# Kernel tuning notes

Measured on AMD Instinct MI355X. Metric: run time of the kernel, lower is better.

## Reference

```python
import jax, jax.numpy as jnp
import numpy as np

D_MODEL = 1024
NUM_HEADS = 16
DEPTH = D_MODEL // NUM_HEADS
B, S = 4, 2048


def setup_inputs() -> dict:
    key = jax.random.key(0)
    ks = jax.random.split(key, 11)
    sc = 1.0 / np.sqrt(D_MODEL)
    return {
        "query": jax.random.normal(ks[0], (B, S, D_MODEL), jnp.float32),
        "key_": jax.random.normal(ks[1], (B, S, D_MODEL), jnp.float32),
        "value": jax.random.normal(ks[2], (B, S, D_MODEL), jnp.float32),
        # torch Linear: y = x @ W.T + b, W shape [out, in]
        "Wq": jax.random.normal(ks[3], (D_MODEL, D_MODEL), jnp.float32) * sc,
        "bq": jax.random.normal(ks[4], (D_MODEL,), jnp.float32) * sc,
        "Wk": jax.random.normal(ks[5], (D_MODEL, D_MODEL), jnp.float32) * sc,
        "bk": jax.random.normal(ks[6], (D_MODEL,), jnp.float32) * sc,
        "Wv": jax.random.normal(ks[7], (D_MODEL, D_MODEL), jnp.float32) * sc,
        "bv": jax.random.normal(ks[8], (D_MODEL,), jnp.float32) * sc,
        "Wo": jax.random.normal(ks[9], (D_MODEL, D_MODEL), jnp.float32) * sc,
        "bo": jax.random.normal(ks[10], (D_MODEL,), jnp.float32) * sc,
    }


def _split_heads(x):
    # [B,S,D] -> [B,H,S,depth]
    b, s, _ = x.shape
    return x.reshape(b, s, NUM_HEADS, DEPTH).transpose(0, 2, 1, 3)


def reference(query, key_, value, Wq, bq, Wk, bk, Wv, bv, Wo, bo):
    Q = _split_heads(query @ Wq.T + bq)
    K = _split_heads(key_ @ Wk.T + bk)
    V = _split_heads(value @ Wv.T + bv)
    scale = 1.0 / jnp.sqrt(jnp.float32(DEPTH))
    scores = jnp.einsum("bhqd,bhkd->bhqk", Q, K) * scale  # [B,H,S,S]
    attention_weights = jax.nn.softmax(scores, axis=-1)
    out = jnp.einsum("bhqk,bhkd->bhqd", attention_weights, V)
    out = out.transpose(0, 2, 1, 3).reshape(query.shape[0], -1, D_MODEL)
    out = out @ Wo.T + bo
    return out, attention_weights
```

## Files before the change

kernel.cpp:

```cpp
#include <hip/hip_runtime.h>

#define NHEAD 16
#define SEQ 2048
#define DMODEL 1024
#define BB 4
#define MROWS (BB*SEQ)
#define NBH (BB*NHEAD)
#define NT (SEQ/32)

typedef float f32x4 __attribute__((ext_vector_type(4)));
typedef _Float16 f16x8 __attribute__((ext_vector_type(8)));
typedef _Float16 f16x4 __attribute__((ext_vector_type(4)));

static __device__ __forceinline__ f32x4 mfma16(f16x8 a, f16x8 b, f32x4 c) {
  return __builtin_amdgcn_mfma_f32_16x16x32_f16(a, b, c, 0, 0, 0);
}

static __device__ __forceinline__ void gload_lds16(const unsigned short* g, unsigned short* l) {
  __builtin_amdgcn_global_load_lds(
      (const __attribute__((address_space(1))) unsigned int*)g,
      (__attribute__((address_space(3))) unsigned int*)l, 16, 0, 0);
}

static __device__ __forceinline__ ushort4 cvt4(float4 x) {
  ushort4 h;
  h.x = __builtin_bit_cast(unsigned short, (_Float16)x.x);
  h.y = __builtin_bit_cast(unsigned short, (_Float16)x.y);
  h.z = __builtin_bit_cast(unsigned short, (_Float16)x.z);
  h.w = __builtin_bit_cast(unsigned short, (_Float16)x.w);
  return h;
}

__global__ __launch_bounds__(256)
void round3_f16(const float* __restrict__ q, const float* __restrict__ k,
                const float* __restrict__ v,
                unsigned short* __restrict__ oq, unsigned short* __restrict__ ok,
                unsigned short* __restrict__ ov, int n4)
{
  const float* src = (blockIdx.y == 0) ? q : (blockIdx.y == 1) ? k : v;
  unsigned short* dst = (blockIdx.y == 0) ? oq : (blockIdx.y == 1) ? ok : ov;
  int i = blockIdx.x*256 + threadIdx.x;
  const int stride = gridDim.x*256;
  for (; i < n4; i += stride)
    ((ushort4*)dst)[i] = cvt4(((const float4*)src)[i]);
}

__global__ __launch_bounds__(256)
void round_w4(const float* __restrict__ w0, const float* __restrict__ w1,
              const float* __restrict__ w2, const float* __restrict__ w3,
              unsigned short* __restrict__ o0, unsigned short* __restrict__ o1,
              unsigned short* __restrict__ o2, unsigned short* __restrict__ o3, int n4)
{
  const float* src = (blockIdx.y == 0) ? w0 : (blockIdx.y == 1) ? w1
                   : (blockIdx.y == 2) ? w2 : w3;
  unsigned short* dst = (blockIdx.y == 0) ? o0 : (blockIdx.y == 1) ? o1
                      : (blockIdx.y == 2) ? o2 : o3;
  int i = blockIdx.x*256 + threadIdx.x;
  const int stride = gridDim.x*256;
  for (; i < n4; i += stride)
    ((ushort4*)dst)[i] = cvt4(((const float4*)src)[i]);
}

static __device__ __forceinline__ void stage_proj(
    unsigned short* ab, unsigned short* bb,
    const unsigned short* __restrict__ Xf, const unsigned short* __restrict__ Wf,
    int m0, int n0, int k0, int tid)
{
#pragma unroll
  for (int r = 0; r < 2; ++r) {
    const int gi = r*256 + tid;
    const int row = gi >> 2, c = gi & 3;
    const int lg = c ^ ((row >> 1) & 3);
    gload_lds16(Xf + (size_t)(m0+row)*DMODEL + k0 + lg*8,
                ab + r*2048 + (tid & 0xC0)*8);
  }
#pragma unroll
  for (int r = 0; r < 2; ++r) {
    const int gi = r*256 + tid;
    const int row = gi >> 2, c = gi & 3;
    const int lg = c ^ ((row >> 1) & 3);
    gload_lds16(Wf + (size_t)(n0+row)*DMODEL + k0 + lg*8,
                bb + r*2048 + (tid & 0xC0)*8);
  }
}

template<int MODE>
__global__ __launch_bounds__(256, 2)
void proj_gemm(const unsigned short* __restrict__ Xf, const unsigned short* __restrict__ Wf,
               const float* __restrict__ bias, float oscale,
               unsigned short* __restrict__ o16, float* __restrict__ o_f32)
{
  __shared__ unsigned short As[2][128][32];
  __shared__ unsigned short Bs[2][128][32];
  const int tid  = threadIdx.x;
  const int wid  = tid >> 6, lane = tid & 63;
  const int g    = lane >> 4, r16 = lane & 15;
  const int id   = blockIdx.y*64 + blockIdx.x;
  const int xcd  = id & 7, slot = id >> 3;
  const int m0   = (xcd*8 + (slot & 7)) * 128;
  const int n0   = (slot >> 3) * 128;
  const int wr   = wid >> 1, wc = wid & 1;

  f32x4 acc[4][4] = {};

  stage_proj(&As[0][0][0], &Bs[0][0][0], Xf, Wf, m0, n0, 0, tid);
  asm volatile("s_waitcnt vmcnt(0)" ::: "memory");
  __builtin_amdgcn_s_barrier();

  for (int kt = 0; kt < 32; ++kt) {
    const int cur = kt & 1;
    if (kt < 31)
      stage_proj(&As[cur^1][0][0], &Bs[cur^1][0][0], Xf, Wf, m0, n0, (kt+1)*32, tid);

    const unsigned short (*Asb)[32] = As[cur];
    const unsigned short (*Bsb)[32] = Bs[cur];
    f16x8 a[4], b[4];
#pragma unroll
    for (int t = 0; t < 4; ++t) {
      const int ar = wr*64 + t*16 + r16;
      a[t] = *(const f16x8*)((const char*)&Asb[ar][0] + ((g ^ ((ar >> 1) & 3)) << 4));
      const int br = wc*64 + t*16 + r16;
      b[t] = *(const f16x8*)((const char*)&Bsb[br][0] + ((g ^ ((br >> 1) & 3)) << 4));
    }
    __builtin_amdgcn_s_setprio(1);
#pragma unroll
    for (int mt = 0; mt < 4; ++mt)
#pragma unroll
      for (int nt = 0; nt < 4; ++nt)
        acc[mt][nt] = mfma16(a[mt], b[nt], acc[mt][nt]);
    __builtin_amdgcn_s_setprio(0);

    if (kt < 31) {
      asm volatile("s_waitcnt vmcnt(0)" ::: "memory");
      __builtin_amdgcn_s_barrier();
    }
  }

#pragma unroll
  for (int nt = 0; nt < 4; ++nt) {
    const int n  = n0 + wc*64 + nt*16 + r16;
    const float bn = bias[n];
#pragma unroll
    for (int mt = 0; mt < 4; ++mt) {
      const int mb = m0 + wr*64 + mt*16 + g*4;
      if (MODE == 0) {
#pragma unroll
        for (int j = 0; j < 4; ++j) {
          const int m = mb + j;
          const int bt = m >> 11, s = m & (SEQ-1);
          const int hh = n >> 6,  d = n & 63;
          o16[(((size_t)(bt*NHEAD + hh)*SEQ + s) << 6) + d] =
              __builtin_bit_cast(unsigned short, (_Float16)((acc[mt][nt][j] + bn) * oscale));
        }
      } else if (MODE == 1) {
        const int bt = mb >> 11, sb = mb & (SEQ-1);
        const int hh = n >> 6,  d = n & 63;
        ushort4 v;
        v.x = __builtin_bit_cast(unsigned short, (_Float16)(acc[mt][nt][0] + bn));
        v.y = __builtin_bit_cast(unsigned short, (_Float16)(acc[mt][nt][1] + bn));
        v.z = __builtin_bit_cast(unsigned short, (_Float16)(acc[mt][nt][2] + bn));
        v.w = __builtin_bit_cast(unsigned short, (_Float16)(acc[mt][nt][3] + bn));
        *(ushort4*)(o16 + ((size_t)(bt*NHEAD + hh)*64 + d)*SEQ + sb) = v;
      } else {
#pragma unroll
        for (int j = 0; j < 4; ++j)
          o_f32[(size_t)(mb + j)*DMODEL + n] = acc[mt][nt][j] + bn;
      }
    }
  }
}

static __device__ __forceinline__ void stage_k(unsigned short* dst,
    const unsigned short* __restrict__ Kf, size_t kbase, int k0, int tid)
{
  const int row = tid >> 3, c = tid & 7;
  const int sg = c ^ (row & 7);
  gload_lds16(Kf + kbase + (size_t)(k0+row)*64 + sg*8, dst + (tid & 0xC0)*8);
}

static __device__ __forceinline__ void stage_v(unsigned short* dst,
    const unsigned short* __restrict__ Vtg, int bh, int k0, int tid)
{
  const int row = tid >> 2, c = tid & 3;
  const int lg = c ^ ((row >> 1) & 3);
  gload_lds16(Vtg + ((size_t)bh*64 + row)*SEQ + k0 + lg*8, dst + (tid & 0xC0)*8);
}

__global__ __launch_bounds__(256, 4)
void attn_fused(const unsigned short* __restrict__ Qf, const unsigned short* __restrict__ Kf,
                const unsigned short* __restrict__ Vtg,
                float* __restrict__ wout, unsigned short* __restrict__ of16)
{
  __shared__ unsigned short Ks[4][32][64];
  __shared__ unsigned short Vs[4][64][32];
  __shared__ unsigned short PA[4][16][40];
  const int tid = threadIdx.x, wid = tid >> 6, lane = tid & 63;
  const int g = lane >> 4, r16 = lane & 15;
  const int id = blockIdx.y*32 + blockIdx.x;
  const int xcd = id & 7, slot = id >> 3;
  const int bh = (slot >> 5)*8 + xcd;
  const int bx = slot & 31;
  const int bt = bh >> 4, hh = bh & (NHEAD-1);
  const int s0 = bx*64 + wid*16;
  const size_t kbase = (size_t)bh*SEQ*64;

  const size_t qoff = ((size_t)bh*SEQ + s0 + r16)*64 + (size_t)g*8;
  const f16x8 qh0 = *(const f16x8*)(Qf + qoff);
  const f16x8 qh1 = *(const f16x8*)(Qf + qoff + 32);

  float lp = 0.f;
  stage_k(&Ks[0][0][0], Kf, kbase, 0, tid);
  stage_k(&Ks[1][0][0], Kf, kbase, 32, tid);
  asm volatile("s_waitcnt vmcnt(1)" ::: "memory");
  __builtin_amdgcn_s_barrier();
  for (int kt = 0; kt < NT; ++kt) {
    const int cur = kt & 3;
    const bool pf = kt < NT-2;
    if (pf) stage_k(&Ks[(kt+2)&3][0][0], Kf, kbase, (kt+2)*32, tid);
#pragma unroll
    for (int sub = 0; sub < 2; ++sub) {
      const int krow = sub*16 + r16;
      const char* pk = (const char*)&Ks[cur][krow][0];
      const int sx = krow & 7;
      const f16x8 kh0 = *(const f16x8*)(pk + (((g    ) ^ sx) << 4));
      const f16x8 kh1 = *(const f16x8*)(pk + (((4 | g) ^ sx) << 4));
      f32x4 acc = {};
      __builtin_amdgcn_s_setprio(1);
      acc = mfma16(kh0, qh0, acc);
      acc = mfma16(kh1, qh1, acc);
      __builtin_amdgcn_s_setprio(0);
#pragma unroll
      for (int j = 0; j < 4; ++j) lp += __builtin_exp2f(acc[j]);
    }
    if (pf) { asm volatile("s_waitcnt vmcnt(1)" ::: "memory"); }
    else    { asm volatile("s_waitcnt vmcnt(0)" ::: "memory"); }
    __builtin_amdgcn_s_barrier();
  }
  lp += __shfl_xor(lp, 16);
  lp += __shfl_xor(lp, 32);
  const float li = 1.0f / lp;

  f32x4 acco[4] = {};
  char* paw = (char*)&PA[wid][0][0];

  stage_k(&Ks[0][0][0], Kf, kbase, 0, tid);
  stage_v(&Vs[0][0][0], Vtg, bh, 0, tid);
  stage_k(&Ks[1][0][0], Kf, kbase, 32, tid);
  stage_v(&Vs[1][0][0], Vtg, bh, 32, tid);
  asm volatile("s_waitcnt vmcnt(2)" ::: "memory");
  __builtin_amdgcn_s_barrier();
  for (int kt = 0; kt < NT; ++kt) {
    const int cur = kt & 3;
    if (kt < NT-2) {
      stage_k(&Ks[(kt+2)&3][0][0], Kf, kbase, (kt+2)*32, tid);
      stage_v(&Vs[(kt+2)&3][0][0], Vtg, bh, (kt+2)*32, tid);
    }
#pragma unroll
    for (int sub = 0; sub < 2; ++sub) {
      const int krow = sub*16 + r16;
      const char* pk = (const char*)&Ks[cur][krow][0];
      const int sx = krow & 7;
      const f16x8 kh0 = *(const f16x8*)(pk + (((g    ) ^ sx) << 4));
      const f16x8 kh1 = *(const f16x8*)(pk + (((4 | g) ^ sx) << 4));
      f32x4 acc = {};
      __builtin_amdgcn_s_setprio(1);
      acc = mfma16(kh0, qh0, acc);
      acc = mfma16(kh1, qh1, acc);
      __builtin_amdgcn_s_setprio(0);
      f32x4 w4;
      f16x4 p4;
#pragma unroll
      for (int j = 0; j < 4; ++j) {
        w4[j] = __builtin_exp2f(acc[j]) * li;
        p4[j] = (_Float16)w4[j];
      }
      float* wp = wout + ((size_t)bh*SEQ + s0 + r16)*SEQ + kt*32 + sub*16 + 4*g;
      __builtin_nontemporal_store(w4, (f32x4*)wp);
      *(f16x4*)(paw + r16*80 + ((((2*sub + (g >> 1)) ^ (r16 & 3)) << 4) | ((g & 1) << 3))) = p4;
    }
    asm volatile("s_waitcnt lgkmcnt(0)" ::: "memory");
    const f16x8 pa = *(const f16x8*)(paw + r16*80 + ((g ^ (r16 & 3)) << 4));
    __builtin_amdgcn_s_setprio(1);
#pragma unroll
    for (int nt = 0; nt < 4; ++nt) {
      const int vrow = nt*16 + r16;
      const f16x8 vv = *(const f16x8*)((const char*)&Vs[cur][vrow][0] +
                                       ((g ^ ((vrow >> 1) & 3)) << 4));
      acco[nt] = mfma16(pa, vv, acco[nt]);
    }
    __builtin_amdgcn_s_setprio(0);
    if (kt == 0) {
      asm volatile("s_waitcnt vmcnt(4)" ::: "memory"); __builtin_amdgcn_s_barrier();
    } else if (kt < NT-2) {
      asm volatile("s_waitcnt vmcnt(6)" ::: "memory"); __builtin_amdgcn_s_barrier();
    } else if (kt == NT-2) {
      asm volatile("s_waitcnt vmcnt(4)" ::: "memory"); __builtin_amdgcn_s_barrier();
    }
  }

#pragma unroll
  for (int nt = 0; nt < 4; ++nt)
#pragma unroll
    for (int j = 0; j < 4; ++j)
      of16[((size_t)bt*SEQ + s0 + 4*g + j)*DMODEL + hh*64 + nt*16 + r16] =
          __builtin_bit_cast(unsigned short, (_Float16)acco[nt][j]);
}

extern "C" void kernel_launch(void* const* d_in, const int* in_sizes, int n_in,
                              void* d_out, int out_size, void* d_ws, size_t ws_size,
                              hipStream_t stream)
{
  const float* query = (const float*)d_in[0];
  const float* key_  = (const float*)d_in[1];
  const float* value = (const float*)d_in[2];
  const float* Wq = (const float*)d_in[3];
  const float* bq = (const float*)d_in[4];
  const float* Wk = (const float*)d_in[5];
  const float* bk = (const float*)d_in[6];
  const float* Wv = (const float*)d_in[7];
  const float* bv = (const float*)d_in[8];
  const float* Wo = (const float*)d_in[9];
  const float* bo = (const float*)d_in[10];

  const size_t NE = (size_t)NBH * SEQ * 64;
  const size_t NW = (size_t)DMODEL * DMODEL;
  unsigned short* Xq16 = (unsigned short*)d_ws;
  unsigned short* Xk16 = Xq16 + NE;
  unsigned short* Xv16 = Xk16 + NE;
  unsigned short* Qf   = Xv16 + NE;
  unsigned short* Kf   = Qf + NE;
  unsigned short* Vt   = Kf + NE;
  unsigned short* Wq16 = Vt + NE;
  unsigned short* Wk16 = Wq16 + NW;
  unsigned short* Wv16 = Wk16 + NW;
  unsigned short* Wo16 = Wv16 + NW;
  unsigned short* Of   = Xq16;

  float* out0  = (float*)d_out;
  float* wattn = out0 + (size_t)MROWS * DMODEL;

  const int nX4 = MROWS*DMODEL/4, nW4 = DMODEL*DMODEL/4;
  const float QSCALE = 0.125f * 1.4426950408889634f;
  dim3 gg(64, 8);

  round3_f16<<<dim3(1024, 3), 256, 0, stream>>>(query, key_, value, Xq16, Xk16, Xv16, nX4);
  round_w4<<<dim3(256, 4), 256, 0, stream>>>(Wq, Wk, Wv, Wo, Wq16, Wk16, Wv16, Wo16, nW4);

  proj_gemm<0><<<gg, dim3(256), 0, stream>>>(Xq16, Wq16, bq, QSCALE, Qf, nullptr);
  proj_gemm<0><<<gg, dim3(256), 0, stream>>>(Xk16, Wk16, bk, 1.0f, Kf, nullptr);
  proj_gemm<1><<<gg, dim3(256), 0, stream>>>(Xv16, Wv16, bv, 1.0f, Vt, nullptr);

  attn_fused<<<dim3(32, NBH), dim3(256), 0, stream>>>(Qf, Kf, Vt, wattn, Of);

  proj_gemm<2><<<gg, dim3(256), 0, stream>>>(Of, Wo16, bo, 1.0f, nullptr, out0);
}
```

Measured before the change: 497.7 us.

## Split attention into row-sum kernel and weights/PV kernel with deeper prefetch

Splits the fused attention kernel into two launches. The first computes the softmax denominators with a 6-stage K buffer at higher occupancy and writes the reciprocal row sums to workspace. The second reads them and deepens the K/V prefetch from 2 to 3 tiles ahead. The aim is to give each pass better latency hiding and occupancy, at the cost of an extra launch and a small global round-trip for the row sums.

```diff
diff --git a/kernel.cpp b/kernel.cpp
--- a/kernel.cpp
+++ b/kernel.cpp
@@ -186,10 +186,66 @@
   gload_lds16(Vtg + ((size_t)bh*64 + row)*SEQ + k0 + lg*8, dst + (tid & 0xC0)*8);
 }
 
+__global__ __launch_bounds__(256, 6)
+void attn_l(const unsigned short* __restrict__ Qf, const unsigned short* __restrict__ Kf,
+            float* __restrict__ lrow)
+{
+  __shared__ unsigned short Ks[6][32][64];
+  const int tid = threadIdx.x, wid = tid >> 6, lane = tid & 63;
+  const int g = lane >> 4, r16 = lane & 15;
+  const int id = blockIdx.y*32 + blockIdx.x;
+  const int xcd = id & 7, slot = id >> 3;
+  const int bh = (slot >> 5)*8 + xcd;
+  const int bx = slot & 31;
+  const int s0 = bx*64 + wid*16;
+  const size_t kbase = (size_t)bh*SEQ*64;
+
+  const size_t qoff = ((size_t)bh*SEQ + s0 + r16)*64 + (size_t)g*8;
+  const f16x8 qh0 = *(const f16x8*)(Qf + qoff);
+  const f16x8 qh1 = *(const f16x8*)(Qf + qoff + 32);
+
+  float lp = 0.f;
+  stage_k(&Ks[0][0][0], Kf, kbase, 0,  tid);
+  stage_k(&Ks[1][0][0], Kf, kbase, 32, tid);
+  stage_k(&Ks[2][0][0], Kf, kbase, 64, tid);
+  stage_k(&Ks[3][0][0], Kf, kbase, 96, tid);
+  asm volatile("s_waitcnt vmcnt(3)" ::: "memory");
+  __builtin_amdgcn_s_barrier();
+
+  int cur = 0, nxt = 4;
+  for (int c = 0; c < NT; ++c) {
+    if (c < NT-4) stage_k(&Ks[nxt][0][0], Kf, kbase, (c+4)*32, tid);
+#pragma unroll
+    for (int sub = 0; sub < 2; ++sub) {
+      const int krow = sub*16 + r16;
+      const char* pk = (const char*)&Ks[cur][krow][0];
+      const int sx = krow & 7;
+      const f16x8 kh0 = *(const f16x8*)(pk + (((g    ) ^ sx) << 4));
+      const f16x8 kh1 = *(const f16x8*)(pk + (((4 | g) ^ sx) << 4));
+      f32x4 acc = {};
+      __builtin_amdgcn_s_setprio(1);
+      acc = mfma16(kh0, qh0, acc);
+      acc = mfma16(kh1, qh1, acc);
+      __builtin_amdgcn_s_setprio(0);
+#pragma unroll
+      for (int j = 0; j < 4; ++j) lp += __builtin_exp2f(acc[j]);
+    }
+    if (c < NT-4)      { asm volatile("s_waitcnt vmcnt(3)" ::: "memory"); __builtin_amdgcn_s_barrier(); }
+    else if (c == NT-4){ asm volatile("s_waitcnt vmcnt(2)" ::: "memory"); __builtin_amdgcn_s_barrier(); }
+    else if (c == NT-3){ asm volatile("s_waitcnt vmcnt(1)" ::: "memory"); __builtin_amdgcn_s_barrier(); }
+    else if (c == NT-2){ asm volatile("s_waitcnt vmcnt(0)" ::: "memory"); __builtin_amdgcn_s_barrier(); }
+    cur = (cur == 5) ? 0 : cur + 1;
+    nxt = (nxt == 5) ? 0 : nxt + 1;
+  }
+  lp += __shfl_xor(lp, 16);
+  lp += __shfl_xor(lp, 32);
+  if (lane < 16) lrow[(size_t)bh*SEQ + s0 + r16] = 1.0f / lp;
+}
+
 __global__ __launch_bounds__(256, 4)
-void attn_fused(const unsigned short* __restrict__ Qf, const unsigned short* __restrict__ Kf,
-                const unsigned short* __restrict__ Vtg,
-                float* __restrict__ wout, unsigned short* __restrict__ of16)
+void attn_wv(const unsigned short* __restrict__ Qf, const unsigned short* __restrict__ Kf,
+             const unsigned short* __restrict__ Vtg, const float* __restrict__ lrow,
+             float* __restrict__ wout, unsigned short* __restrict__ of16)
 {
   __shared__ unsigned short Ks[4][32][64];
   __shared__ unsigned short Vs[4][64][32];
@@ -207,38 +263,7 @@
   const size_t qoff = ((size_t)bh*SEQ + s0 + r16)*64 + (size_t)g*8;
   const f16x8 qh0 = *(const f16x8*)(Qf + qoff);
   const f16x8 qh1 = *(const f16x8*)(Qf + qoff + 32);
-
-  float lp = 0.f;
-  stage_k(&Ks[0][0][0], Kf, kbase, 0, tid);
-  stage_k(&Ks[1][0][0], Kf, kbase, 32, tid);
-  asm volatile("s_waitcnt vmcnt(1)" ::: "memory");
-  __builtin_amdgcn_s_barrier();
-  for (int kt = 0; kt < NT; ++kt) {
-    const int cur = kt & 3;
-    const bool pf = kt < NT-2;
-    if (pf) stage_k(&Ks[(kt+2)&3][0][0], Kf, kbase, (kt+2)*32, tid);
-#pragma unroll
-    for (int sub = 0; sub < 2; ++sub) {
-      const int krow = sub*16 + r16;
-      const char* pk = (const char*)&Ks[cur][krow][0];
-      const int sx = krow & 7;
-      const f16x8 kh0 = *(const f16x8*)(pk + (((g    ) ^ sx) << 4));
-      const f16x8 kh1 = *(const f16x8*)(pk + (((4 | g) ^ sx) << 4));
-      f32x4 acc = {};
-      __builtin_amdgcn_s_setprio(1);
-      acc = mfma16(kh0, qh0, acc);
-      acc = mfma16(kh1, qh1, acc);
-      __builtin_amdgcn_s_setprio(0);
-#pragma unroll
-      for (int j = 0; j < 4; ++j) lp += __builtin_exp2f(acc[j]);
-    }
-    if (pf) { asm volatile("s_waitcnt vmcnt(1)" ::: "memory"); }
-    else    { asm volatile("s_waitcnt vmcnt(0)" ::: "memory"); }
-    __builtin_amdgcn_s_barrier();
-  }
-  lp += __shfl_xor(lp, 16);
-  lp += __shfl_xor(lp, 32);
-  const float li = 1.0f / lp;
+  const float li = lrow[(size_t)bh*SEQ + s0 + r16];
 
   f32x4 acco[4] = {};
   char* paw = (char*)&PA[wid][0][0];
@@ -247,13 +272,16 @@
   stage_v(&Vs[0][0][0], Vtg, bh, 0, tid);
   stage_k(&Ks[1][0][0], Kf, kbase, 32, tid);
   stage_v(&Vs[1][0][0], Vtg, bh, 32, tid);
-  asm volatile("s_waitcnt vmcnt(2)" ::: "memory");
+  stage_k(&Ks[2][0][0], Kf, kbase, 64, tid);
+  stage_v(&Vs[2][0][0], Vtg, bh, 64, tid);
+  asm volatile("s_waitcnt vmcnt(4)" ::: "memory");
   __builtin_amdgcn_s_barrier();
+
   for (int kt = 0; kt < NT; ++kt) {
     const int cur = kt & 3;
-    if (kt < NT-2) {
-      stage_k(&Ks[(kt+2)&3][0][0], Kf, kbase, (kt+2)*32, tid);
-      stage_v(&Vs[(kt+2)&3][0][0], Vtg, bh, (kt+2)*32, tid);
+    if (kt < NT-3) {
+      stage_k(&Ks[(kt+3)&3][0][0], Kf, kbase, (kt+3)*32, tid);
+      stage_v(&Vs[(kt+3)&3][0][0], Vtg, bh, (kt+3)*32, tid);
     }
 #pragma unroll
     for (int sub = 0; sub < 2; ++sub) {
@@ -289,13 +317,11 @@
       acco[nt] = mfma16(pa, vv, acco[nt]);
     }
     __builtin_amdgcn_s_setprio(0);
-    if (kt == 0) {
-      asm volatile("s_waitcnt vmcnt(4)" ::: "memory"); __builtin_amdgcn_s_barrier();
-    } else if (kt < NT-2) {
-      asm volatile("s_waitcnt vmcnt(6)" ::: "memory"); __builtin_amdgcn_s_barrier();
-    } else if (kt == NT-2) {
-      asm volatile("s_waitcnt vmcnt(4)" ::: "memory"); __builtin_amdgcn_s_barrier();
-    }
+    if (kt == 0)          { asm volatile("s_waitcnt vmcnt(6)"  ::: "memory"); __builtin_amdgcn_s_barrier(); }
+    else if (kt == 1)     { asm volatile("s_waitcnt vmcnt(8)"  ::: "memory"); __builtin_amdgcn_s_barrier(); }
+    else if (kt < NT-3)   { asm volatile("s_waitcnt vmcnt(10)" ::: "memory"); __builtin_amdgcn_s_barrier(); }
+    else if (kt == NT-3)  { asm volatile("s_waitcnt vmcnt(8)"  ::: "memory"); __builtin_amdgcn_s_barrier(); }
+    else if (kt == NT-2)  { asm volatile("s_waitcnt vmcnt(6)"  ::: "memory"); __builtin_amdgcn_s_barrier(); }
   }
 
 #pragma unroll
@@ -334,6 +360,7 @@
   unsigned short* Wk16 = Wq16 + NW;
   unsigned short* Wv16 = Wk16 + NW;
   unsigned short* Wo16 = Wv16 + NW;
+  float* lrow          = (float*)(Wo16 + NW);
   unsigned short* Of   = Xq16;
 
   float* out0  = (float*)d_out;
@@ -350,7 +377,8 @@
   proj_gemm<0><<<gg, dim3(256), 0, stream>>>(Xk16, Wk16, bk, 1.0f, Kf, nullptr);
   proj_gemm<1><<<gg, dim3(256), 0, stream>>>(Xv16, Wv16, bv, 1.0f, Vt, nullptr);
 
-  attn_fused<<<dim3(32, NBH), dim3(256), 0, stream>>>(Qf, Kf, Vt, wattn, Of);
+  attn_l <<<dim3(32, NBH), dim3(256), 0, stream>>>(Qf, Kf, lrow);
+  attn_wv<<<dim3(32, NBH), dim3(256), 0, stream>>>(Qf, Kf, Vt, lrow, wattn, Of);
 
   proj_gemm<2><<<gg, dim3(256), 0, stream>>>(Of, Wo16, bo, 1.0f, nullptr, out0);
 }
```

Result: slower. 576.5 us (+15.8%).
